# Optimization experiments

Measured on AMD Instinct MI355X. Metric: run time of the kernel, lower is better.

## Reference

```python
import jax, jax.numpy as jnp
import numpy as np

SEQ, BATCH, IN, HID, OUT = 512, 64, 512, 1024, 512
KEEP = 0.7  # dropout p = 0.3


def setup_inputs() -> dict:
    key = jax.random.key(0)
    ks = jax.random.split(key, 9)
    def lin(k, fan_out, fan_in):
        bound = 1.0 / np.sqrt(fan_in)
        kw, kb = jax.random.split(k)
        W = jax.random.uniform(kw, (fan_out, fan_in), jnp.float32, -bound, bound)
        b = jax.random.uniform(kb, (fan_out,), jnp.float32, -bound, bound)
        return W, b
    x = jax.random.normal(ks[0], (SEQ, BATCH, IN), jnp.float32)
    # inverted dropout mask, fixed for determinism
    drop_mask = (jax.random.bernoulli(ks[1], KEEP, (SEQ, BATCH, OUT))
                 .astype(jnp.float32) / KEEP)
    W_i2h, b_i2h = lin(ks[2], HID, IN + HID)
    W_i2o, b_i2o = lin(ks[3], OUT, IN + HID)
    W_o2o, b_o2o = lin(ks[4], OUT, HID + OUT)
    return {"x": x, "drop_mask": drop_mask,
            "W_i2h": W_i2h, "b_i2h": b_i2h,
            "W_i2o": W_i2o, "b_i2o": b_i2o,
            "W_o2o": W_o2o, "b_o2o": b_o2o}


def reference(x, drop_mask, W_i2h, b_i2h, W_i2o, b_i2o, W_o2o, b_o2o):
    # x: [S, B, IN]; returns log-probs [S, B, OUT]
    def step(h, inp):
        x_t, m_t = inp  # [B, IN], [B, OUT]
        comb = jnp.concatenate([x_t, h], axis=1)          # [B, IN+HID]
        out = comb @ W_i2o.T + b_i2o                      # [B, OUT]
        h_new = comb @ W_i2h.T + b_i2h                    # [B, HID]
        oc = jnp.concatenate([out, h_new], axis=1) @ W_o2o.T + b_o2o  # [B, OUT]
        oc = oc * m_t                                     # dropout (inverted mask)
        oc = jax.nn.log_softmax(oc, axis=-1)
        return h_new, oc
    h0 = jnp.zeros((x.shape[1], W_i2h.shape[0]), x.dtype)
    _, outs = jax.lax.scan(step, h0, (x, drop_mask))
    return outs
```

## Files before the change

kernel.cpp:

```cpp
#include <hip/hip_runtime.h>
#include <stdint.h>


typedef unsigned short ushort_t;
typedef __attribute__((ext_vector_type(8))) __bf16 bf16x8;
typedef __attribute__((ext_vector_type(4))) float f32x4;

__device__ __forceinline__ ushort_t f2bf(float f) {
  union { float f; uint32_t u; } v; v.f = f;
  uint32_t r = v.u + 0x7fffu + ((v.u >> 16) & 1u);
  return (ushort_t)(r >> 16);
}
__device__ __forceinline__ float bf2f(ushort_t b) {
  union { uint32_t u; float f; } v; v.u = ((uint32_t)b) << 16;
  return v.f;
}
__device__ __forceinline__ void gload16(const ushort_t* g, ushort_t* l) {
  __builtin_amdgcn_global_load_lds(
      (const __attribute__((address_space(1))) uint32_t*)g,
      (__attribute__((address_space(3))) uint32_t*)l, 16, 0, 0);
}

__global__ __launch_bounds__(256) void init_kernel(uint32_t* harr0) {
  int i = blockIdx.x * blockDim.x + threadIdx.x;
  if (i < 32768) harr0[i] = 0;
}

__global__ __launch_bounds__(256) void pack_kernel(
    const float* __restrict__ x, const float* __restrict__ mask,
    const float* __restrict__ W_i2h,
    const float* __restrict__ W_i2o, const float* __restrict__ W_o2o,
    const float* __restrict__ b_i2o, const float* __restrict__ b_o2o,
    ushort_t* xB, ushort_t* Wihx, ushort_t* Whh, ushort_t* Wiox,
    ushort_t* Wioh, ushort_t* Wo1, ushort_t* Wo2, float* biasP,
    uint64_t* maskb) {
  int64_t i = (int64_t)blockIdx.x * blockDim.x + threadIdx.x;
  const int64_t c0 = 16777216, c1 = 17301504, c2 = 18350080, c3 = 18612224,
                c4 = 19136512, c5 = 19398656, c6 = 19922944, c7 = 19923456,
                c8 = 36700672;
  if (i < c0) { xB[i] = f2bf(x[i]); return; }
  if (i < c1) { int64_t j = i - c0; int r = j >> 9,  c = j & 511;  Wihx[j] = f2bf(W_i2h[(int64_t)r * 1536 + c]); return; }
  if (i < c2) { int64_t j = i - c1; int r = j >> 10, c = j & 1023; Whh[j]  = f2bf(W_i2h[(int64_t)r * 1536 + 512 + c]); return; }
  if (i < c3) { int64_t j = i - c2; int r = j >> 9,  c = j & 511;  Wiox[j] = f2bf(W_i2o[(int64_t)r * 1536 + c]); return; }
  if (i < c4) { int64_t j = i - c3; int r = j >> 10, c = j & 1023; Wioh[j] = f2bf(W_i2o[(int64_t)r * 1536 + 512 + c]); return; }
  if (i < c5) { int64_t j = i - c4; int r = j >> 9,  c = j & 511;  Wo1[j]  = f2bf(W_o2o[(int64_t)r * 1536 + c]); return; }
  if (i < c6) { int64_t j = i - c5; int r = j >> 10, c = j & 1023; Wo2[j]  = f2bf(W_o2o[(int64_t)r * 1536 + 512 + c]); return; }
  if (i < c7) {
    int n = (int)(i - c6);
    const float* wr = W_o2o + (int64_t)n * 1536;
    float s = 0.f;
    for (int m = 0; m < 512; ++m) s += wr[m] * b_i2o[m];
    biasP[n] = s + b_o2o[n];
    return;
  }
  if (i < c8) {
    int64_t j = i - c7;
    float v = mask[j];
    uint64_t bits = __ballot(v != 0.0f);
    if ((j & 63) == 0) maskb[j >> 6] = bits;
  }
}

__device__ void usetup_tile(ushort_t* SH,
    const ushort_t* __restrict__ Wo1, const ushort_t* __restrict__ Wiox,
    const ushort_t* __restrict__ Wioh, ushort_t* __restrict__ U1,
    ushort_t* __restrict__ U2, int job) {
  ushort_t* AsF = SH;
  ushort_t* BsF = SH + 4096;
  const ushort_t* Bm; ushort_t* Om; int mt, nt, ldb;
  if (job < 16) { mt = job >> 2; nt = job & 3; Bm = Wiox; Om = U1; ldb = 512; }
  else { job -= 16; mt = job >> 3; nt = job & 7; Bm = Wioh; Om = U2; ldb = 1024; }
  const int m0 = mt * 128, n0 = nt * 128;
  const int tid = threadIdx.x;
  const int w = tid >> 6, l = tid & 63;
  const int quad = l >> 4, l15 = l & 15;
  const int wm = (w & 1) * 64, wn = (w >> 1) * 64;
  const int r0 = tid >> 2, chunk = tid & 3;
  f32x4 acc[4][4] = {};
  for (int k0 = 0; k0 < 512; k0 += 32) {
    __syncthreads();
    gload16(Wo1 + (size_t)(m0 + r0) * 512 + k0 + chunk * 8,      &AsF[tid * 8]);
    gload16(Wo1 + (size_t)(m0 + r0 + 64) * 512 + k0 + chunk * 8, &AsF[2048 + tid * 8]);
#pragma unroll
    for (int rep = 0; rep < 2; ++rep) {
      const int idx = tid + 256 * rep;
      const int kk = idx & 31, n8 = idx >> 5;
      union { uint4 v; ushort_t s[8]; } u;
      u.v = *(const uint4*)(Bm + (size_t)(k0 + kk) * ldb + n0 + n8 * 8);
#pragma unroll
      for (int i = 0; i < 8; ++i) BsF[(n8 * 8 + i) * 32 + kk] = u.s[i];
    }
    __syncthreads();
    bf16x8 af[4], bfr[4];
#pragma unroll
    for (int i = 0; i < 4; ++i) af[i]  = *(const bf16x8*)&AsF[(wm + 16 * i + l15) * 32 + 8 * quad];
#pragma unroll
    for (int j = 0; j < 4; ++j) bfr[j] = *(const bf16x8*)&BsF[(wn + 16 * j + l15) * 32 + 8 * quad];
#pragma unroll
    for (int i = 0; i < 4; ++i)
#pragma unroll
      for (int j = 0; j < 4; ++j)
        acc[i][j] = __builtin_amdgcn_mfma_f32_16x16x32_bf16(af[i], bfr[j], acc[i][j], 0, 0, 0);
  }
#pragma unroll
  for (int i = 0; i < 4; ++i) {
    const int row = m0 + wm + 16 * i + 4 * quad;
#pragma unroll
    for (int j = 0; j < 4; ++j) {
      const int col = n0 + wn + 16 * j + l15;
#pragma unroll
      for (int r = 0; r < 4; ++r)
        Om[(size_t)(row + r) * ldb + col] = f2bf(acc[i][j][r]);
    }
  }
}

__global__ __launch_bounds__(256) void gemm_bt(
    const ushort_t* __restrict__ A1, int lda1, const ushort_t* __restrict__ B1, int K1,
    const float* __restrict__ bias, ushort_t* Cb, int Ntiles,
    const ushort_t* __restrict__ Wo1, const ushort_t* __restrict__ Wiox,
    const ushort_t* __restrict__ Wioh, ushort_t* __restrict__ U1,
    ushort_t* __restrict__ U2) {
  __shared__ __align__(16) ushort_t SH[16384];
  if (blockIdx.x >= 2048) {
    usetup_tile(SH, Wo1, Wiox, Wioh, U1, U2, blockIdx.x - 2048);
    return;
  }
  const int mt = blockIdx.x & 255, nt = blockIdx.x >> 8;
  const int m0 = mt * 128, n0 = nt * 128;
  const int tid = threadIdx.x;
  const int w = tid >> 6, l = tid & 63;
  const int quad = l >> 4, l15 = l & 15;
  const int wm = (w & 1) * 64, wn = (w >> 1) * 64;
  const int r0 = tid >> 2, chunk = tid & 3;
  f32x4 acc[4][4] = {};
  gload16(A1 + (size_t)(m0 + r0) * lda1 + chunk * 8,      &SH[tid * 8]);
  gload16(A1 + (size_t)(m0 + r0 + 64) * lda1 + chunk * 8, &SH[2048 + tid * 8]);
  gload16(B1 + (size_t)(n0 + r0) * K1 + chunk * 8,        &SH[8192 + tid * 8]);
  gload16(B1 + (size_t)(n0 + r0 + 64) * K1 + chunk * 8,   &SH[8192 + 2048 + tid * 8]);
  const int NIT = K1 >> 5;
  for (int it = 0; it < NIT; ++it) {
    const int p = it & 1;
    const int ao = p * 4096, bo = 8192 + p * 4096;
    __syncthreads();
    if (it + 1 < NIT) {
      const int kn = (it + 1) * 32;
      const int an = (p ^ 1) * 4096, bn = 8192 + (p ^ 1) * 4096;
      gload16(A1 + (size_t)(m0 + r0) * lda1 + kn + chunk * 8,      &SH[an + tid * 8]);
      gload16(A1 + (size_t)(m0 + r0 + 64) * lda1 + kn + chunk * 8, &SH[an + 2048 + tid * 8]);
      gload16(B1 + (size_t)(n0 + r0) * K1 + kn + chunk * 8,        &SH[bn + tid * 8]);
      gload16(B1 + (size_t)(n0 + r0 + 64) * K1 + kn + chunk * 8,   &SH[bn + 2048 + tid * 8]);
    }
    bf16x8 af[4], bfr[4];
#pragma unroll
    for (int i = 0; i < 4; ++i) af[i]  = *(const bf16x8*)&SH[ao + (wm + 16 * i + l15) * 32 + 8 * quad];
#pragma unroll
    for (int j = 0; j < 4; ++j) bfr[j] = *(const bf16x8*)&SH[bo + (wn + 16 * j + l15) * 32 + 8 * quad];
#pragma unroll
    for (int i = 0; i < 4; ++i)
#pragma unroll
      for (int j = 0; j < 4; ++j)
        acc[i][j] = __builtin_amdgcn_mfma_f32_16x16x32_bf16(af[i], bfr[j], acc[i][j], 0, 0, 0);
  }
  const int N = Ntiles * 128;
#pragma unroll
  for (int i = 0; i < 4; ++i) {
    const int row = m0 + wm + 16 * i + 4 * quad;
#pragma unroll
    for (int j = 0; j < 4; ++j) {
      const int col = n0 + wn + 16 * j + l15;
      const float bv = bias[col];
#pragma unroll
      for (int r = 0; r < 4; ++r)
        Cb[(size_t)(row + r) * N + col] = f2bf(acc[i][j][r] + bv);
    }
  }
}

template<int NTERMS>
__device__ void pair_tile128T(ushort_t* SH,
    const ushort_t* __restrict__ A0r0, const ushort_t* __restrict__ A0r1,
    const ushort_t* __restrict__ B0,
    const ushort_t* __restrict__ A1r0, const ushort_t* __restrict__ A1r1,
    const ushort_t* __restrict__ B1,
    int n0, const ushort_t* __restrict__ Xh, ushort_t* __restrict__ Oh,
    int gate) {
  const int tid = threadIdx.x;
  const int w = tid >> 6, l = tid & 63;
  const int quad = l >> 4, l15 = l & 15;
  const int wm = (w & 1) * 64, wn = (w >> 1) * 64;
  const int r0 = tid >> 2, chunk = tid & 3;
  const int thrA  = r0 * 1024 + chunk * 8;
  const int thrB0 = (n0 + r0) * 1024 + chunk * 8;
  const int thrB1 = (n0 + r0 + 64) * 1024 + chunk * 8;
  const ushort_t* ga0 = A0r0 + thrA;
  const ushort_t* ga1 = A0r1 + thrA;
  const ushort_t* gb0 = B0 + thrB0;
  const ushort_t* gb1 = B0 + thrB1;
  f32x4 acc[4][4] = {};
  gload16(ga0, &SH[tid * 8]);
  gload16(ga1, &SH[2048 + tid * 8]);
  gload16(gb0, &SH[8192 + tid * 8]);
  gload16(gb1, &SH[8192 + 2048 + tid * 8]);
  const int NIT = NTERMS * 32;
  for (int it = 0; it < NIT; ++it) {
    const int p = it & 1;
    const int ap = p * 4096, bp = 8192 + p * 4096;
    __syncthreads();
    if (it + 1 < NIT) {
      if (NTERMS == 2 && it == 31) {
        ga0 = A1r0 + thrA; ga1 = A1r1 + thrA;
        gb0 = B1 + thrB0;  gb1 = B1 + thrB1;
      } else {
        ga0 += 32; ga1 += 32; gb0 += 32; gb1 += 32;
      }
      const int an = (p ^ 1) * 4096, bn = 8192 + (p ^ 1) * 4096;
      gload16(ga0, &SH[an + tid * 8]);
      gload16(ga1, &SH[an + 2048 + tid * 8]);
      gload16(gb0, &SH[bn + tid * 8]);
      gload16(gb1, &SH[bn + 2048 + tid * 8]);
    }
    bf16x8 af[4], bfr[4];
#pragma unroll
    for (int i = 0; i < 4; ++i) af[i]  = *(const bf16x8*)&SH[ap + (wm + 16 * i + l15) * 32 + 8 * quad];
#pragma unroll
    for (int j = 0; j < 4; ++j) bfr[j] = *(const bf16x8*)&SH[bp + (wn + 16 * j + l15) * 32 + 8 * quad];
#pragma unroll
    for (int i = 0; i < 4; ++i)
#pragma unroll
      for (int j = 0; j < 4; ++j)
        acc[i][j] = __builtin_amdgcn_mfma_f32_16x16x32_bf16(af[i], bfr[j], acc[i][j], 0, 0, 0);
  }
#pragma unroll
  for (int i = 0; i < 4; ++i) {
#pragma unroll
    for (int j = 0; j < 4; ++j) {
      const int col = n0 + wn + 16 * j + l15;
#pragma unroll
      for (int r = 0; r < 4; ++r) {
        const int lrow = 16 * i + 4 * quad + r;
        const size_t idx = (size_t)lrow * 1024 + col;
        float v = gate ? acc[i][j][r] : 0.0f;
        Oh[idx] = f2bf(v + bf2f(Xh[idx]));
      }
    }
  }
}

__device__ void copy_tile(const ushort_t* X, ushort_t* O, int n0) {
  const int t = threadIdx.x, r = t >> 2, q = t & 3;
  const uint4* src = (const uint4*)(X + (size_t)r * 1024 + n0 + q * 32);
  uint4* dst = (uint4*)(O + (size_t)r * 1024 + n0 + q * 32);
  dst[0] = src[0]; dst[1] = src[1]; dst[2] = src[2]; dst[3] = src[3];
}

__device__ void power_tile(ushort_t* SH,
                           const ushort_t* __restrict__ Am,
                           const ushort_t* __restrict__ Bm,
                           ushort_t* __restrict__ Om, int t) {
  ushort_t* AsF = SH;
  ushort_t* BsF = SH + 4096;
  const int mt = t & 7, nt = (t >> 3) & 7;
  const int m0 = mt * 128, n0 = nt * 128;
  const int tid = threadIdx.x;
  const int w = tid >> 6, l = tid & 63;
  const int quad = l >> 4, l15 = l & 15;
  const int wm = (w & 1) * 64, wn = (w >> 1) * 64;
  const int r0 = tid >> 2, chunk = tid & 3;
  f32x4 acc[4][4] = {};
  for (int k0 = 0; k0 < 1024; k0 += 32) {
    __syncthreads();
    gload16(Am + (size_t)(m0 + r0) * 1024 + k0 + chunk * 8,      &AsF[tid * 8]);
    gload16(Am + (size_t)(m0 + r0 + 64) * 1024 + k0 + chunk * 8, &AsF[2048 + tid * 8]);
#pragma unroll
    for (int rep = 0; rep < 2; ++rep) {
      const int idx = tid + 256 * rep;
      const int kk = idx & 31, n8 = idx >> 5;
      union { uint4 v; ushort_t s[8]; } u;
      u.v = *(const uint4*)(Bm + (size_t)(k0 + kk) * 1024 + n0 + n8 * 8);
#pragma unroll
      for (int i = 0; i < 8; ++i) BsF[(n8 * 8 + i) * 32 + kk] = u.s[i];
    }
    __syncthreads();
    bf16x8 af[4], bfr[4];
#pragma unroll
    for (int i = 0; i < 4; ++i) af[i]  = *(const bf16x8*)&AsF[(wm + 16 * i + l15) * 32 + 8 * quad];
#pragma unroll
    for (int j = 0; j < 4; ++j) bfr[j] = *(const bf16x8*)&BsF[(wn + 16 * j + l15) * 32 + 8 * quad];
#pragma unroll
    for (int i = 0; i < 4; ++i)
#pragma unroll
      for (int j = 0; j < 4; ++j)
        acc[i][j] = __builtin_amdgcn_mfma_f32_16x16x32_bf16(af[i], bfr[j], acc[i][j], 0, 0, 0);
  }
#pragma unroll
  for (int i = 0; i < 4; ++i) {
    const int row = m0 + wm + 16 * i + 4 * quad;
#pragma unroll
    for (int j = 0; j < 4; ++j) {
      const int col = n0 + wn + 16 * j + l15;
#pragma unroll
      for (int r = 0; r < 4; ++r)
        Om[(size_t)(row + r) * 1024 + col] = f2bf(acc[i][j][r]);
    }
  }
}

#define PWp(idx) (Pw + (size_t)(idx) * 1048576)

__global__ __launch_bounds__(256) void pass_kernel(
    const ushort_t* __restrict__ XhB, ushort_t* __restrict__ Harr,
    const ushort_t* __restrict__ Whh, ushort_t* __restrict__ Pw, int mode) {
  __shared__ __align__(16) ushort_t SH[16384];
  const int bid = blockIdx.x;
  const int npow = (mode == 1) ? 64 : ((mode == 2) ? 128 : 256);
  if (bid < npow) {
    const int pj = bid >> 6, t = bid & 63;
    const ushort_t *Am, *Bm; ushort_t* Om;
    if (mode == 1)      { Am = Whh;    Bm = Whh;    Om = PWp(0); }
    else if (mode == 2) {
      if (pj == 0) { Am = Whh;    Bm = PWp(0); Om = PWp(1); }
      else         { Am = PWp(0); Bm = PWp(0); Om = PWp(2); }
    } else {
      switch (pj) {
        case 0:  Am = Whh;    Bm = PWp(2); Om = PWp(3); break;
        case 1:  Am = PWp(0); Bm = PWp(2); Om = PWp(4); break;
        case 2:  Am = PWp(1); Bm = PWp(2); Om = PWp(5); break;
        default: Am = PWp(2); Bm = PWp(2); Om = PWp(6); break;
      }
    }
    power_tile(SH, Am, Bm, Om, t);
    return;
  }
  const int inner0 = bid - npow;
  const int u = inner0 >> 8, inner = inner0 & 255;
  const int p_ = (inner & 7) | (((inner >> 6) & 3) << 3);
  const int n0 = ((inner >> 3) & 7) * 128;
#define HS_(s) (Harr + (size_t)(s) * 65536)
#define XS_(s) (XhB + (size_t)(s) * 65536)
  const ushort_t *A0, *B0, *A1 = nullptr, *B1 = nullptr, *X; ushort_t* O;
  int terms = 1;
  if (mode == 1) {
    const int as[4] = {0, 2, 4, 6}, xs[4] = {1, 3, 5, 7}, os[4] = {2, 4, 1, 8};
    A0 = XS_(as[u]); B0 = Whh; X = XS_(xs[u]); O = HS_(os[u]);
  } else if (mode == 2) {
    if (u == 0)      { A0 = HS_(2); B0 = Whh;    X = XS_(2); O = HS_(3); }
    else if (u == 1) { A0 = HS_(2); B0 = PWp(0); X = HS_(4); O = HS_(4); }
    else             { A0 = HS_(1); B0 = PWp(0); X = HS_(8); O = HS_(8); }
  } else {
    if (u == 0)      { A0 = HS_(4); B0 = Whh;    X = XS_(4); O = HS_(5); }
    else if (u == 1) { A0 = HS_(4); B0 = PWp(0); X = HS_(1); O = HS_(6); }
    else if (u == 2) { A0 = HS_(1); B0 = Whh; A1 = HS_(4); B1 = PWp(1);
                       terms = 2;               X = XS_(6); O = HS_(7); }
    else             { A0 = HS_(4); B0 = PWp(2); X = HS_(8); O = HS_(8); }
  }
  const size_t co0 = (size_t)(2 * p_) * 524288;
  const size_t co1 = co0 + 524288;
  const int half = (threadIdx.x >> 6) & 1;
  const size_t coh = half ? co1 : co0;
  if (terms == 2)
    pair_tile128T<2>(SH, A0 + co0, A0 + co1, B0, A1 + co0, A1 + co1, B1,
                     n0, X + coh, O + coh, 1);
  else
    pair_tile128T<1>(SH, A0 + co0, A0 + co1, B0, nullptr, nullptr, nullptr,
                     n0, X + coh, O + coh, 1);
}

__global__ __launch_bounds__(256) void scan64(
    const ushort_t* __restrict__ old, ushort_t* __restrict__ nw,
    const ushort_t* __restrict__ Pv, int d,
    const ushort_t* __restrict__ Pra, ushort_t* __restrict__ Pwo, int nride) {
  __shared__ __align__(16) ushort_t SH[16384];
  if (blockIdx.x < nride) {
    power_tile(SH, Pra, Pra, Pwo, blockIdx.x);
    return;
  }
  const int bid = blockIdx.x - nride;
  const int p_ = (bid & 7) | (((bid >> 6) & 3) << 3);
  const int n0 = ((bid >> 3) & 7) * 128;
  const int c0 = 2 * p_, c1 = c0 + 1;
  if (c1 < d) {
    copy_tile(old + (size_t)c0 * 524288, nw + (size_t)c0 * 524288, n0);
    copy_tile(old + (size_t)c1 * 524288, nw + (size_t)c1 * 524288, n0);
    return;
  }
  const int ia0 = (c0 >= d) ? (c0 - d) : 0;
  const int ia1 = c1 - d;
  const int half = (threadIdx.x >> 6) & 1;
  const int ch = half ? c1 : c0;
  const int gate = (ch >= d);
  pair_tile128T<1>(SH, old + (size_t)ia0 * 524288, old + (size_t)ia1 * 524288,
                   Pv, nullptr, nullptr, nullptr, n0,
                   old + (size_t)ch * 524288, nw + (size_t)ch * 524288, gate);
}

__global__ __launch_bounds__(256) void correct_kernel(
    const ushort_t* __restrict__ S, const ushort_t* __restrict__ XhB,
    ushort_t* __restrict__ Harr, const ushort_t* __restrict__ Whh,
    const ushort_t* __restrict__ Pw) {
  __shared__ __align__(16) ushort_t SH[16384];
  const int bx = blockIdx.x;
  const int p_ = (bx & 7) | ((bx >> 6) << 3);
  const int n0 = ((bx >> 3) & 7) * 128;
  const int j = blockIdx.y + 1;
  const ushort_t* Wj = (j == 1) ? Whh : (Pw + (size_t)(j - 2) * 1048576);
  const ushort_t* Xs = (j == 1) ? XhB : (Harr + (size_t)j * 65536);
  ushort_t* XO = Harr + (size_t)j * 65536;
  const size_t co0 = (size_t)(2 * p_) * 524288;
  const size_t co1 = co0 + 524288;
  const int half = (threadIdx.x >> 6) & 1;
  const size_t coh = half ? co1 : co0;
  pair_tile128T<1>(SH, S + co0, S + co1, Wj, nullptr, nullptr, nullptr,
                   n0, Xs + coh, XO + coh, 1);
}

__global__ __launch_bounds__(256) void gemm_fused(
    const ushort_t* __restrict__ xB, const ushort_t* __restrict__ U1,
    const ushort_t* __restrict__ Harr, const ushort_t* __restrict__ U2,
    const ushort_t* __restrict__ Wo2, const float* __restrict__ biasP,
    const uint64_t* __restrict__ maskb, float* __restrict__ out) {
  __shared__ __align__(16) ushort_t AsF[2][4096];
  __shared__ __align__(16) ushort_t BsF[2][4096];
  const int mt = blockIdx.x & 255, nt = blockIdx.x >> 8;
  const int m0 = mt * 128, n0 = nt * 128;
  const int tid = threadIdx.x;
  const int w = tid >> 6, l = tid & 63;
  const int quad = l >> 4, l15 = l & 15;
  const int wm = (w & 1) * 64, wn = (w >> 1) * 64;
  const int r0 = tid >> 2, chunk = tid & 3;
  f32x4 acc[4][4] = {};
  auto issue = [&](int it, int b) {
    const ushort_t *A, *B; int K, k0;
    if (it < 16)      { A = xB;           B = U1;  K = 512;  k0 = it << 5; }
    else if (it < 48) { A = Harr;         B = U2;  K = 1024; k0 = (it - 16) << 5; }
    else              { A = Harr + 65536; B = Wo2; K = 1024; k0 = (it - 48) << 5; }
    gload16(A + (size_t)(m0 + r0) * K + k0 + chunk * 8,      &AsF[b][tid * 8]);
    gload16(A + (size_t)(m0 + r0 + 64) * K + k0 + chunk * 8, &AsF[b][2048 + tid * 8]);
    gload16(B + (size_t)(n0 + r0) * K + k0 + chunk * 8,      &BsF[b][tid * 8]);
    gload16(B + (size_t)(n0 + r0 + 64) * K + k0 + chunk * 8, &BsF[b][2048 + tid * 8]);
  };
  issue(0, 0);
  for (int it = 0; it < 80; ++it) {
    const int p = it & 1;
    __syncthreads();
    if (it < 79) issue(it + 1, p ^ 1);
    bf16x8 af[4], bfr[4];
#pragma unroll
    for (int i = 0; i < 4; ++i) af[i]  = *(const bf16x8*)&AsF[p][(wm + 16 * i + l15) * 32 + 8 * quad];
#pragma unroll
    for (int j = 0; j < 4; ++j) bfr[j] = *(const bf16x8*)&BsF[p][(wn + 16 * j + l15) * 32 + 8 * quad];
#pragma unroll
    for (int i = 0; i < 4; ++i)
#pragma unroll
      for (int j = 0; j < 4; ++j)
        acc[i][j] = __builtin_amdgcn_mfma_f32_16x16x32_bf16(af[i], bfr[j], acc[i][j], 0, 0, 0);
  }
  const float INV_KEEP = 1.0f / 0.7f;
#pragma unroll
  for (int i = 0; i < 4; ++i) {
    const int row = m0 + wm + 16 * i + 4 * quad;
#pragma unroll
    for (int j = 0; j < 4; ++j) {
      const int col = n0 + wn + 16 * j + l15;
      const float bv = biasP[col];
#pragma unroll
      for (int r = 0; r < 4; ++r) {
        const size_t idx = (size_t)(row + r) * 512 + col;
        const uint64_t bits = maskb[idx >> 6];
        out[idx] = ((bits >> (idx & 63)) & 1) ? (acc[i][j][r] + bv) * INV_KEEP
                                              : 0.0f;
      }
    }
  }
}

__global__ __launch_bounds__(256) void softmax_kernel(float* __restrict__ out) {
  const int row = blockIdx.x;
  const int tid = threadIdx.x;
  const size_t base = (size_t)row * 512;
  __shared__ float sm[4], ss[4];
  const float v0 = out[base + tid];
  const float v1 = out[base + tid + 256];
  float m = fmaxf(v0, v1);
#pragma unroll
  for (int off = 32; off; off >>= 1) m = fmaxf(m, __shfl_xor(m, off, 64));
  const int w = tid >> 6;
  if ((tid & 63) == 0) sm[w] = m;
  __syncthreads();
  m = fmaxf(fmaxf(sm[0], sm[1]), fmaxf(sm[2], sm[3]));
  float s = __expf(v0 - m) + __expf(v1 - m);
#pragma unroll
  for (int off = 32; off; off >>= 1) s += __shfl_xor(s, off, 64);
  if ((tid & 63) == 0) ss[w] = s;
  __syncthreads();
  s = ss[0] + ss[1] + ss[2] + ss[3];
  const float lg = logf(s);
  out[base + tid] = v0 - m - lg;
  out[base + tid + 256] = v1 - m - lg;
}

extern "C" void kernel_launch(void* const* d_in, const int* in_sizes, int n_in,
                              void* d_out, int out_size, void* d_ws, size_t ws_size,
                              hipStream_t stream) {
  const float* x     = (const float*)d_in[0];
  const float* mask  = (const float*)d_in[1];
  const float* W_i2h = (const float*)d_in[2];
  const float* b_i2h = (const float*)d_in[3];
  const float* W_i2o = (const float*)d_in[4];
  const float* b_i2o = (const float*)d_in[5];
  const float* W_o2o = (const float*)d_in[6];
  const float* b_o2o = (const float*)d_in[7];
  float* out = (float*)d_out;

  char* ws = (char*)d_ws;
  const size_t NEED = 207749120;
  if (ws_size < NEED) return;
  ushort_t* xB   = (ushort_t*)(ws + 0);
  ushort_t* XhB  = (ushort_t*)(ws + 33554432);
  ushort_t* SA   = XhB + 65536;
  ushort_t* SB   = XhB + 3 * 65536;
  ushort_t* Harr = (ushort_t*)(ws + 100663296);
  ushort_t* Pw   = (ushort_t*)(ws + 167903232);
  ushort_t* U1   = (ushort_t*)(ws + 193069056);
  ushort_t* U2   = (ushort_t*)(ws + 193593344);
  float* biasP   = (float*)(ws + 194641920);
  uint64_t* maskb = (uint64_t*)(ws + 195000320);
  ushort_t* Wihx = (ushort_t*)(ws + 201457664);
  ushort_t* Whh  = (ushort_t*)(ws + 202506240);
  ushort_t* Wiox = (ushort_t*)(ws + 204603392);
  ushort_t* Wioh = (ushort_t*)(ws + 205127680);
  ushort_t* Wo1  = (ushort_t*)(ws + 206176256);
  ushort_t* Wo2  = (ushort_t*)(ws + 206700544);

  hipLaunchKernelGGL(init_kernel, dim3(128), dim3(256), 0, stream, (uint32_t*)Harr);
  hipLaunchKernelGGL(pack_kernel, dim3(143362), dim3(256), 0, stream,
                     x, mask, W_i2h, W_i2o, W_o2o, b_i2o, b_o2o,
                     xB, Wihx, Whh, Wiox, Wioh, Wo1, Wo2, biasP, maskb);
  hipLaunchKernelGGL(gemm_bt, dim3(2096), dim3(256), 0, stream,
                     xB, 512, Wihx, 512, b_i2h, XhB, 8,
                     Wo1, Wiox, Wioh, U1, U2);
  hipLaunchKernelGGL(pass_kernel, dim3(1088), dim3(256), 0, stream,
                     XhB, Harr, Whh, Pw, 1);
  hipLaunchKernelGGL(pass_kernel, dim3(896), dim3(256), 0, stream,
                     XhB, Harr, Whh, Pw, 2);
  hipLaunchKernelGGL(pass_kernel, dim3(1280), dim3(256), 0, stream,
                     XhB, Harr, Whh, Pw, 3);
  hipLaunchKernelGGL(scan64, dim3(320), dim3(256), 0, stream, Harr, SB, PWp(6),  1, PWp(6),  PWp(7),  64);
  hipLaunchKernelGGL(scan64, dim3(320), dim3(256), 0, stream, SB, SA, PWp(7),  2, PWp(7),  PWp(8),  64);
  hipLaunchKernelGGL(scan64, dim3(320), dim3(256), 0, stream, SA, SB, PWp(8),  4, PWp(8),  PWp(9),  64);
  hipLaunchKernelGGL(scan64, dim3(320), dim3(256), 0, stream, SB, SA, PWp(9),  8, PWp(9),  PWp(10), 64);
  hipLaunchKernelGGL(scan64, dim3(320), dim3(256), 0, stream, SA, SB, PWp(10), 16, PWp(10), PWp(11), 64);
  hipLaunchKernelGGL(scan64, dim3(256), dim3(256), 0, stream, SB, SA, PWp(11), 32, (const ushort_t*)nullptr, (ushort_t*)nullptr, 0);
  hipLaunchKernelGGL(correct_kernel, dim3(dim3(256, 8)), dim3(256), 0, stream,
                     SA, XhB, Harr, Whh, Pw);
  hipLaunchKernelGGL(gemm_fused, dim3(1024), dim3(256), 0, stream,
                     xB, U1, Harr, U2, Wo2, biasP, maskb, out);
  hipLaunchKernelGGL(softmax_kernel, dim3(32768), dim3(256), 0, stream, out);
}
```

Measured before the change: 1.158 ms.

## Fold init into pack kernel, parallelize bias dot, inline double-buffered correct GEMM

Removes the separate Harr zero-init launch by folding it into pack_kernel, and rewrites the per-row bias projection as a wavefront-parallel reduction with shuffle adds instead of a serial 512-element loop per thread. The correct_kernel is rewritten from the shared pair_tile128T helper into an inline double-buffered MFMA GEMM with direct global-to-LDS loads and a simpler block-to-tile mapping. These changes aim to cut launch overhead, a long serial tail in pack, and pipeline stalls in the correction pass, at the cost of duplicated GEMM code and a changed block order.

```diff
diff --git a/kernel.cpp b/kernel.cpp
--- a/kernel.cpp
+++ b/kernel.cpp
@@ -19,11 +19,6 @@
   __builtin_amdgcn_global_load_lds(
       (const __attribute__((address_space(1))) uint32_t*)g,
       (__attribute__((address_space(3))) uint32_t*)l, 16, 0, 0);
-}
-
-__global__ __launch_bounds__(256) void init_kernel(uint32_t* harr0) {
-  int i = blockIdx.x * blockDim.x + threadIdx.x;
-  if (i < 32768) harr0[i] = 0;
 }
 
 __global__ __launch_bounds__(256) void pack_kernel(
@@ -33,11 +28,13 @@
     const float* __restrict__ b_i2o, const float* __restrict__ b_o2o,
     ushort_t* xB, ushort_t* Wihx, ushort_t* Whh, ushort_t* Wiox,
     ushort_t* Wioh, ushort_t* Wo1, ushort_t* Wo2, float* biasP,
-    uint64_t* maskb) {
+    uint64_t* maskb, uint32_t* harr0) {
   int64_t i = (int64_t)blockIdx.x * blockDim.x + threadIdx.x;
   const int64_t c0 = 16777216, c1 = 17301504, c2 = 18350080, c3 = 18612224,
-                c4 = 19136512, c5 = 19398656, c6 = 19922944, c7 = 19923456,
-                c8 = 36700672;
+                c4 = 19136512, c5 = 19398656, c6 = 19922944,
+                cB = 19955712,
+                cM = 36732928,
+                cI = 36765696;
   if (i < c0) { xB[i] = f2bf(x[i]); return; }
   if (i < c1) { int64_t j = i - c0; int r = j >> 9,  c = j & 511;  Wihx[j] = f2bf(W_i2h[(int64_t)r * 1536 + c]); return; }
   if (i < c2) { int64_t j = i - c1; int r = j >> 10, c = j & 1023; Whh[j]  = f2bf(W_i2h[(int64_t)r * 1536 + 512 + c]); return; }
@@ -45,19 +42,30 @@
   if (i < c4) { int64_t j = i - c3; int r = j >> 10, c = j & 1023; Wioh[j] = f2bf(W_i2o[(int64_t)r * 1536 + 512 + c]); return; }
   if (i < c5) { int64_t j = i - c4; int r = j >> 9,  c = j & 511;  Wo1[j]  = f2bf(W_o2o[(int64_t)r * 1536 + c]); return; }
   if (i < c6) { int64_t j = i - c5; int r = j >> 10, c = j & 1023; Wo2[j]  = f2bf(W_o2o[(int64_t)r * 1536 + 512 + c]); return; }
-  if (i < c7) {
-    int n = (int)(i - c6);
+  if (i < cB) {
+    int64_t q = i - c6;
+    const int n = (int)(q >> 6), lane = (int)(q & 63);
     const float* wr = W_o2o + (int64_t)n * 1536;
     float s = 0.f;
-    for (int m = 0; m < 512; ++m) s += wr[m] * b_i2o[m];
-    biasP[n] = s + b_o2o[n];
+#pragma unroll
+    for (int k = 0; k < 8; ++k) {
+      const int m = lane + 64 * k;
+      s += wr[m] * b_i2o[m];
+    }
+#pragma unroll
+    for (int off = 32; off; off >>= 1) s += __shfl_xor(s, off, 64);
+    if (lane == 0) biasP[n] = s + b_o2o[n];
     return;
   }
-  if (i < c8) {
-    int64_t j = i - c7;
+  if (i < cM) {
+    int64_t j = i - cB;
     float v = mask[j];
     uint64_t bits = __ballot(v != 0.0f);
     if ((j & 63) == 0) maskb[j >> 6] = bits;
+    return;
+  }
+  if (i < cI) {
+    harr0[i - cM] = 0;
   }
 }
 
@@ -398,20 +406,61 @@
     const ushort_t* __restrict__ S, const ushort_t* __restrict__ XhB,
     ushort_t* __restrict__ Harr, const ushort_t* __restrict__ Whh,
     const ushort_t* __restrict__ Pw) {
-  __shared__ __align__(16) ushort_t SH[16384];
-  const int bx = blockIdx.x;
-  const int p_ = (bx & 7) | ((bx >> 6) << 3);
-  const int n0 = ((bx >> 3) & 7) * 128;
+  __shared__ __align__(16) ushort_t AsF[2][4096];
+  __shared__ __align__(16) ushort_t BsF[2][4096];
+  const int p_ = blockIdx.x >> 3;
+  const int n0 = (blockIdx.x & 7) * 128;
   const int j = blockIdx.y + 1;
   const ushort_t* Wj = (j == 1) ? Whh : (Pw + (size_t)(j - 2) * 1048576);
   const ushort_t* Xs = (j == 1) ? XhB : (Harr + (size_t)j * 65536);
   ushort_t* XO = Harr + (size_t)j * 65536;
-  const size_t co0 = (size_t)(2 * p_) * 524288;
-  const size_t co1 = co0 + 524288;
-  const int half = (threadIdx.x >> 6) & 1;
-  const size_t coh = half ? co1 : co0;
-  pair_tile128T<1>(SH, S + co0, S + co1, Wj, nullptr, nullptr, nullptr,
-                   n0, Xs + coh, XO + coh, 1);
+  const int tid = threadIdx.x;
+  const int w = tid >> 6, l = tid & 63;
+  const int quad = l >> 4, l15 = l & 15;
+  const int wm = (w & 1) * 64, wn = (w >> 1) * 64;
+  const int r0 = tid >> 2, chunk = tid & 3;
+  f32x4 acc[4][4] = {};
+  const ushort_t* a0 = S + (size_t)(2 * p_) * 524288 + (size_t)r0 * 1024;
+  const ushort_t* a1 = S + (size_t)(2 * p_ + 1) * 524288 + (size_t)r0 * 1024;
+  gload16(a0 + chunk * 8, &AsF[0][tid * 8]);
+  gload16(a1 + chunk * 8, &AsF[0][2048 + tid * 8]);
+  gload16(Wj + (size_t)(n0 + r0) * 1024 + chunk * 8,      &BsF[0][tid * 8]);
+  gload16(Wj + (size_t)(n0 + r0 + 64) * 1024 + chunk * 8, &BsF[0][2048 + tid * 8]);
+  for (int it = 0; it < 32; ++it) {
+    const int p = it & 1;
+    __syncthreads();
+    if (it < 31) {
+      const int kn = (it + 1) * 32;
+      gload16(a0 + kn + chunk * 8, &AsF[p ^ 1][tid * 8]);
+      gload16(a1 + kn + chunk * 8, &AsF[p ^ 1][2048 + tid * 8]);
+      gload16(Wj + (size_t)(n0 + r0) * 1024 + kn + chunk * 8,      &BsF[p ^ 1][tid * 8]);
+      gload16(Wj + (size_t)(n0 + r0 + 64) * 1024 + kn + chunk * 8, &BsF[p ^ 1][2048 + tid * 8]);
+    }
+    bf16x8 af[4], bfr[4];
+#pragma unroll
+    for (int i = 0; i < 4; ++i) af[i]  = *(const bf16x8*)&AsF[p][(wm + 16 * i + l15) * 32 + 8 * quad];
+#pragma unroll
+    for (int jj = 0; jj < 4; ++jj) bfr[jj] = *(const bf16x8*)&BsF[p][(wn + 16 * jj + l15) * 32 + 8 * quad];
+#pragma unroll
+    for (int i = 0; i < 4; ++i)
+#pragma unroll
+      for (int jj = 0; jj < 4; ++jj)
+        acc[i][jj] = __builtin_amdgcn_mfma_f32_16x16x32_bf16(af[i], bfr[jj], acc[i][jj], 0, 0, 0);
+  }
+#pragma unroll
+  for (int i = 0; i < 4; ++i) {
+#pragma unroll
+    for (int jj = 0; jj < 4; ++jj) {
+      const int col = n0 + wn + 16 * jj + l15;
+#pragma unroll
+      for (int r = 0; r < 4; ++r) {
+        const int gr = wm + 16 * i + 4 * quad + r;
+        const int c = 2 * p_ + (gr >> 6);
+        const size_t idx = (size_t)c * 524288 + (size_t)(gr & 63) * 1024 + col;
+        XO[idx] = f2bf(acc[i][jj][r] + bf2f(Xs[idx]));
+      }
+    }
+  }
 }
 
 __global__ __launch_bounds__(256) void gemm_fused(
@@ -532,10 +581,10 @@
   ushort_t* Wo1  = (ushort_t*)(ws + 206176256);
   ushort_t* Wo2  = (ushort_t*)(ws + 206700544);
 
-  hipLaunchKernelGGL(init_kernel, dim3(128), dim3(256), 0, stream, (uint32_t*)Harr);
-  hipLaunchKernelGGL(pack_kernel, dim3(143362), dim3(256), 0, stream,
+  hipLaunchKernelGGL(pack_kernel, dim3(143616), dim3(256), 0, stream,
                      x, mask, W_i2h, W_i2o, W_o2o, b_i2o, b_o2o,
-                     xB, Wihx, Whh, Wiox, Wioh, Wo1, Wo2, biasP, maskb);
+                     xB, Wihx, Whh, Wiox, Wioh, Wo1, Wo2, biasP, maskb,
+                     (uint32_t*)Harr);
   hipLaunchKernelGGL(gemm_bt, dim3(2096), dim3(256), 0, stream,
                      xB, 512, Wihx, 512, b_i2h, XhB, 8,
                      Wo1, Wiox, Wioh, U1, U2);
```

After: 1.113 ms. 1.04x faster.
